# Kernel tuning notes

Measured on AMD Instinct MI355X. Metric: run time of the kernel, lower is better.

Reference implementation:

```python
import jax, jax.numpy as jnp
import numpy as np

# Dimensions (production-scale Qwen3-MoE-like, scaled for CPU exec)
T = 1024   # num_tokens
H = 1024   # hidden_size
F = 768    # moe_inter_padding_size (per-expert ffn dim)
E = 32     # expert_num (== num_local_experts, ep_size=1 -> expert_map is identity)
K = 4      # moe_k (top-k)


def setup_inputs() -> dict:
    key = jax.random.key(0)
    k1, k2, k3, k4 = jax.random.split(key, 4)
    hidden_states = jax.random.normal(k1, (T, H), jnp.float32)
    gate_w = jax.random.normal(k2, (E, H), jnp.float32) * 0.02       # router Linear weight (out,in)
    w1 = jax.random.normal(k3, (E, 2 * F, H), jnp.float32) * 0.02    # fused gate+up proj per expert
    w2 = jax.random.normal(k4, (E, H, F), jnp.float32) * 0.02        # down proj per expert
    return {"hidden_states": hidden_states, "gate_w": gate_w, "w1": w1, "w2": w2}


def reference(hidden_states, gate_w, w1, w2):
    # Router gate (logits computed in fp32, as in the torch code)
    router_logits = (hidden_states @ gate_w.T).astype(jnp.float32)      # [T, E]
    probs = jax.nn.softmax(router_logits, axis=-1)                      # [T, E]
    # SelectTopkOp: top-k over softmax probs, renormalize selected weights
    topk_w, topk_ids = jax.lax.top_k(probs, K)                          # [T, K]
    topk_w = topk_w / jnp.sum(topk_w, axis=-1, keepdims=True)
    # Dense combine weights: cw[t, e] = sum_k topk_w[t, k] * [topk_ids[t, k] == e]
    onehot = jax.nn.one_hot(topk_ids, E, dtype=topk_w.dtype)            # [T, K, E]
    cw = jnp.einsum("tk,tke->te", topk_w, onehot)                       # [T, E]
    # Grouped expert MLP with SiGLU: silu(gate) * up, then down proj
    gu = jnp.einsum("th,egh->etg", hidden_states, w1)                   # [E, T, 2F]
    g, u = gu[..., :F], gu[..., F:]
    act = jax.nn.silu(g) * u                                            # [E, T, F]
    y = jnp.einsum("etf,ehf->eth", act, w2)                             # [E, T, H]
    # Combine: weight each expert's output by its (sparse) routing weight
    out = jnp.einsum("eth,te->th", y, cw.astype(y.dtype))               # [T, H]
    return out
```

## Files before the change

kernel.cpp:

```cpp
#include <hip/hip_runtime.h>
#include <hip/hip_bf16.h>
#include <cmath>

#define TT 1024
#define HH 1024
#define FF 768
#define EE 32
#define MAXTILE 96

typedef __bf16 bf16;
typedef __bf16 v4bf __attribute__((ext_vector_type(4)));
typedef __bf16 v8bf __attribute__((ext_vector_type(8)));
typedef float  v4f  __attribute__((ext_vector_type(4)));

static __device__ __forceinline__ v4f mfma16(v8bf a, v8bf b, v4f c) {
    return __builtin_amdgcn_mfma_f32_16x16x32_bf16(a, b, c, 0, 0, 0);
}

__global__ __launch_bounds__(64) void router_k(
    const float* __restrict__ x, const float* __restrict__ gw,
    bf16* __restrict__ xbf, int* __restrict__ tk_id, float* __restrict__ tk_w)
{
    int t = blockIdx.x, lane = threadIdx.x;
    float4 xr[4];
    const float4* xrow = (const float4*)(x + (size_t)t * HH);
#pragma unroll
    for (int i = 0; i < 4; ++i) xr[i] = xrow[i * 64 + lane];
#pragma unroll
    for (int i = 0; i < 4; ++i) {
        v4bf b = { (bf16)xr[i].x, (bf16)xr[i].y, (bf16)xr[i].z, (bf16)xr[i].w };
        *(v4bf*)(xbf + (size_t)t * HH + (i * 64 + lane) * 4) = b;
    }

    double acc[EE];
#pragma unroll
    for (int e = 0; e < EE; ++e) {
        const float4* grow = (const float4*)(gw + (size_t)e * HH);
        double a = 0.0;
#pragma unroll
        for (int i = 0; i < 4; ++i) {
            float4 g = grow[i * 64 + lane];
            a += (double)xr[i].x * g.x + (double)xr[i].y * g.y
               + (double)xr[i].z * g.z + (double)xr[i].w * g.w;
        }
        acc[e] = a;
    }
#pragma unroll
    for (int m = 1; m < 64; m <<= 1) {
#pragma unroll
        for (int e = 0; e < EE; ++e) acc[e] += __shfl_xor(acc[e], m, 64);
    }
    if (lane == 0) {
        int ids[4]; double lv[4];
        for (int k = 0; k < 4; ++k) {
            int best = 0; double bv = -1.0e300;
            for (int e = 0; e < EE; ++e)
                if (acc[e] > bv) { bv = acc[e]; best = e; }
            ids[k] = best; lv[k] = bv; acc[best] = -2.0e300;
        }
        double w[4], s = 0.0;
        for (int k = 0; k < 4; ++k) { w[k] = exp(lv[k] - lv[0]); s += w[k]; }
        for (int k = 0; k < 4; ++k) {
            tk_id[t * 4 + k] = ids[k];
            tk_w[t * 4 + k] = (float)(w[k] / s);
        }
    }
}

__global__ __launch_bounds__(1024) void scatter_k(
    const int* __restrict__ tk_id, const float* __restrict__ tk_w,
    int* __restrict__ cnt, int* __restrict__ offs,
    int* __restrict__ list, float* __restrict__ wlist,
    int* __restrict__ tile_e, int* __restrict__ tile_m)
{
    __shared__ int c_s[EE], o_s[EE], cur_s[EE];
    int tid = threadIdx.x;
    if (tid < EE) { c_s[tid] = 0; cur_s[tid] = 0; }
    __syncthreads();
    int ids[4]; float w[4];
#pragma unroll
    for (int k = 0; k < 4; ++k) { ids[k] = tk_id[tid * 4 + k]; w[k] = tk_w[tid * 4 + k]; }
#pragma unroll
    for (int k = 0; k < 4; ++k) atomicAdd(&c_s[ids[k]], 1);
    __syncthreads();
    if (tid == 0) {
        int a = 0;
        for (int e = 0; e < EE; ++e) { o_s[e] = a; a += c_s[e]; }
        int nt = 0;
        for (int e = 0; e < EE; ++e)
            for (int m = 0; m * 64 < c_s[e]; ++m) { tile_e[nt] = e; tile_m[nt] = m; ++nt; }
        for (int i = nt; i < MAXTILE; ++i) { tile_e[i] = -1; tile_m[i] = 0; }
    }
    __syncthreads();
#pragma unroll
    for (int k = 0; k < 4; ++k) {
        int e = ids[k];
        int pos = atomicAdd(&cur_s[e], 1);
        int idx = o_s[e] + pos;
        list[idx] = tid * 4 + k;
        wlist[idx] = w[k];
    }
    if (tid < EE) { cnt[tid] = c_s[tid]; offs[tid] = o_s[tid]; }
    if (tid >= 1024 - 64) {
        list[4096 + (tid - 960)] = 0;
        wlist[4096 + (tid - 960)] = 0.f;
    }
}

__global__ __launch_bounds__(256) void gemm1_k(
    const bf16* __restrict__ xbf, const float* __restrict__ w1,
    const int* __restrict__ cnt, const int* __restrict__ offs,
    const int* __restrict__ list, const int* __restrict__ tile_e,
    const int* __restrict__ tile_m, bf16* __restrict__ act)
{
    int id = blockIdx.x;
    int p = (id & 7) * 144 + (id >> 3);
    int fb = p / MAXTILE, tl = p % MAXTILE;
    int e = tile_e[tl];
    if (e < 0) return;
    int mt = tile_m[tl];
    int n = cnt[e];
    int base = offs[e];

    __shared__ bf16 As[64][72];
    __shared__ bf16 Bs[128][72];

    int tid = threadIdx.x;
    int wid = tid >> 6, lane = tid & 63;
    int wr = wid >> 1, wc = wid & 1;
    int lrow = lane & 15, lk = (lane >> 4) * 8;
    const float* w1e = w1 + (size_t)e * 1536 * HH;

    int r0 = tid >> 3, r1 = 32 + (tid >> 3), oct = tid & 7;
    int tk0 = list[base + mt * 64 + r0] >> 2;
    int tk1 = list[base + mt * 64 + r1] >> 2;

    v4f accg[2][2], accu[2][2];
#pragma unroll
    for (int m = 0; m < 2; ++m)
#pragma unroll
        for (int nf = 0; nf < 2; ++nf) { accg[m][nf] = (v4f)0.f; accu[m][nf] = (v4f)0.f; }

    for (int k0 = 0; k0 < HH; k0 += 64) {
        *(v8bf*)&As[r0][oct * 8] = *(const v8bf*)(xbf + (size_t)tk0 * HH + k0 + oct * 8);
        *(v8bf*)&As[r1][oct * 8] = *(const v8bf*)(xbf + (size_t)tk1 * HH + k0 + oct * 8);
#pragma unroll
        for (int it = 0; it < 8; ++it) {
            int r = it * 16 + (tid >> 4);
            int q = tid & 15;
            int grow = (r < 64) ? (fb * 64 + r) : (768 + fb * 64 + (r - 64));
            float4 v = *(const float4*)(w1e + (size_t)grow * HH + k0 + q * 4);
            bf16* dst = &Bs[r][q * 4];
            dst[0] = (bf16)v.x; dst[1] = (bf16)v.y;
            dst[2] = (bf16)v.z; dst[3] = (bf16)v.w;
        }
        __syncthreads();
#pragma unroll
        for (int ks = 0; ks < 2; ++ks) {
            int kk = ks * 32 + lk;
            v8bf a0  = *(const v8bf*)&As[wr * 32 + lrow][kk];
            v8bf a1  = *(const v8bf*)&As[wr * 32 + 16 + lrow][kk];
            v8bf bg0 = *(const v8bf*)&Bs[wc * 32 + lrow][kk];
            v8bf bg1 = *(const v8bf*)&Bs[wc * 32 + 16 + lrow][kk];
            v8bf bu0 = *(const v8bf*)&Bs[64 + wc * 32 + lrow][kk];
            v8bf bu1 = *(const v8bf*)&Bs[64 + wc * 32 + 16 + lrow][kk];
            accg[0][0] = mfma16(a0, bg0, accg[0][0]);
            accg[0][1] = mfma16(a0, bg1, accg[0][1]);
            accg[1][0] = mfma16(a1, bg0, accg[1][0]);
            accg[1][1] = mfma16(a1, bg1, accg[1][1]);
            accu[0][0] = mfma16(a0, bu0, accu[0][0]);
            accu[0][1] = mfma16(a0, bu1, accu[0][1]);
            accu[1][0] = mfma16(a1, bu0, accu[1][0]);
            accu[1][1] = mfma16(a1, bu1, accu[1][1]);
        }
        __syncthreads();
    }
    int rb = wr * 32 + (lane >> 4) * 4;
#pragma unroll
    for (int m = 0; m < 2; ++m)
#pragma unroll
        for (int nf = 0; nf < 2; ++nf)
#pragma unroll
            for (int j = 0; j < 4; ++j) {
                int r = mt * 64 + rb + m * 16 + j;
                if (r < n) {
                    float g = accg[m][nf][j], u = accu[m][nf][j];
                    float a = g / (1.f + __expf(-g)) * u;
                    act[(size_t)(base + r) * FF + fb * 64 + wc * 32 + nf * 16 + lrow] = (bf16)a;
                }
            }
}

__global__ __launch_bounds__(256) void gemm2_k(
    const bf16* __restrict__ act, const float* __restrict__ w2,
    const int* __restrict__ cnt, const int* __restrict__ offs,
    const int* __restrict__ list, const float* __restrict__ wlist,
    const int* __restrict__ tile_e, const int* __restrict__ tile_m,
    float* __restrict__ ybuf)
{
    int id = blockIdx.x;
    int p = (id & 7) * 192 + (id >> 3);
    int hb = p / MAXTILE, tl = p % MAXTILE;
    int e = tile_e[tl];
    if (e < 0) return;
    int mt = tile_m[tl];
    int n = cnt[e];
    int base = offs[e];

    __shared__ bf16 As[64][72];
    __shared__ bf16 Bs[64][72];

    int tid = threadIdx.x;
    int wid = tid >> 6, lane = tid & 63;
    int wr = wid >> 1, wc = wid & 1;
    int lrow = lane & 15, lk = (lane >> 4) * 8;
    const float* w2e = w2 + (size_t)e * HH * FF;

    int r0 = tid >> 3, r1 = 32 + (tid >> 3), oct = tid & 7;
    const bf16* arow0 = act + (size_t)(base + mt * 64 + r0) * FF;
    const bf16* arow1 = act + (size_t)(base + mt * 64 + r1) * FF;

    v4f acc[2][2];
#pragma unroll
    for (int m = 0; m < 2; ++m)
#pragma unroll
        for (int nf = 0; nf < 2; ++nf) acc[m][nf] = (v4f)0.f;

    for (int k0 = 0; k0 < FF; k0 += 64) {
        *(v8bf*)&As[r0][oct * 8] = *(const v8bf*)(arow0 + k0 + oct * 8);
        *(v8bf*)&As[r1][oct * 8] = *(const v8bf*)(arow1 + k0 + oct * 8);
#pragma unroll
        for (int it = 0; it < 4; ++it) {
            int r = it * 16 + (tid >> 4);
            int q = tid & 15;
            float4 v = *(const float4*)(w2e + (size_t)(hb * 64 + r) * FF + k0 + q * 4);
            bf16* dst = &Bs[r][q * 4];
            dst[0] = (bf16)v.x; dst[1] = (bf16)v.y;
            dst[2] = (bf16)v.z; dst[3] = (bf16)v.w;
        }
        __syncthreads();
#pragma unroll
        for (int ks = 0; ks < 2; ++ks) {
            int kk = ks * 32 + lk;
            v8bf a0 = *(const v8bf*)&As[wr * 32 + lrow][kk];
            v8bf a1 = *(const v8bf*)&As[wr * 32 + 16 + lrow][kk];
            v8bf b0 = *(const v8bf*)&Bs[wc * 32 + lrow][kk];
            v8bf b1 = *(const v8bf*)&Bs[wc * 32 + 16 + lrow][kk];
            acc[0][0] = mfma16(a0, b0, acc[0][0]);
            acc[0][1] = mfma16(a0, b1, acc[0][1]);
            acc[1][0] = mfma16(a1, b0, acc[1][0]);
            acc[1][1] = mfma16(a1, b1, acc[1][1]);
        }
        __syncthreads();
    }
    int rb = wr * 32 + (lane >> 4) * 4;
#pragma unroll
    for (int m = 0; m < 2; ++m)
#pragma unroll
        for (int j = 0; j < 4; ++j) {
            int r = mt * 64 + rb + m * 16 + j;
            if (r < n) {
                int code = list[base + r];
                float w = wlist[base + r];
#pragma unroll
                for (int nf = 0; nf < 2; ++nf) {
                    int col = wc * 32 + nf * 16 + lrow;
                    ybuf[(size_t)code * HH + hb * 64 + col] = acc[m][nf][j] * w;
                }
            }
        }
}

__global__ __launch_bounds__(256) void combine_k(
    const float* __restrict__ ybuf, float* __restrict__ out)
{
    int idx = blockIdx.x * 256 + threadIdx.x;
    int t = idx >> 8, c = idx & 255;
    const float4* yb = (const float4*)ybuf;
    float4 a = yb[(size_t)(t * 4 + 0) * 256 + c];
    float4 b = yb[(size_t)(t * 4 + 1) * 256 + c];
    float4 d = yb[(size_t)(t * 4 + 2) * 256 + c];
    float4 e = yb[(size_t)(t * 4 + 3) * 256 + c];
    float4 s;
    s.x = a.x + b.x + d.x + e.x;
    s.y = a.y + b.y + d.y + e.y;
    s.z = a.z + b.z + d.z + e.z;
    s.w = a.w + b.w + d.w + e.w;
    ((float4*)out)[(size_t)t * 256 + c] = s;
}

extern "C" void kernel_launch(void* const* d_in, const int* in_sizes, int n_in,
                              void* d_out, int out_size, void* d_ws, size_t ws_size,
                              hipStream_t stream)
{
    const float* x  = (const float*)d_in[0];
    const float* gw = (const float*)d_in[1];
    const float* w1 = (const float*)d_in[2];
    const float* w2 = (const float*)d_in[3];
    float* out = (float*)d_out;

    char* ws = (char*)d_ws;
    size_t off = 0;
    auto alloc = [&](size_t bytes) {
        void* p = ws + off;
        off = (off + bytes + 255) & ~(size_t)255;
        return p;
    };
    bf16*  xbf    = (bf16*) alloc((size_t)TT * HH * 2);
    int*   tk_id  = (int*)  alloc(4096 * 4);
    float* tk_w   = (float*)alloc(4096 * 4);
    int*   cnt    = (int*)  alloc(EE * 4);
    int*   offs   = (int*)  alloc(EE * 4);
    int*   list   = (int*)  alloc(4160 * 4);
    float* wlist  = (float*)alloc(4160 * 4);
    int*   tile_e = (int*)  alloc(MAXTILE * 4);
    int*   tile_m = (int*)  alloc(MAXTILE * 4);
    bf16*  act    = (bf16*) alloc((size_t)4160 * FF * 2);
    float* ybuf   = (float*)alloc((size_t)4096 * HH * 4);

    router_k<<<TT, 64, 0, stream>>>(x, gw, xbf, tk_id, tk_w);
    scatter_k<<<1, 1024, 0, stream>>>(tk_id, tk_w, cnt, offs, list, wlist, tile_e, tile_m);
    gemm1_k<<<MAXTILE * 12, 256, 0, stream>>>(xbf, w1, cnt, offs, list, tile_e, tile_m, act);
    gemm2_k<<<MAXTILE * 16, 256, 0, stream>>>(act, w2, cnt, offs, list, wlist, tile_e, tile_m, ybuf);
    combine_k<<<1024, 256, 0, stream>>>(ybuf, out);
}
```

Before: 482.2 us.

## Prefetch next K-tile into registers, reorder tile mapping, atomic-add combine into output

Both grouped GEMMs now load the next K-slice of activations and weights into registers before running the MFMAs on the current slice, then write it to shared memory, so global load latency overlaps compute. The block-to-tile mapping changes so that consecutive blocks share the same expert tile and sweep its F/H column blocks instead of the reverse. The per-slot ybuf plus combine kernel is replaced by zeroing the output and having gemm2 atomically add weighted results into it, which removes a large intermediate write and read but introduces atomic contention and non-deterministic summation order.

```diff
diff --git a/kernel.cpp b/kernel.cpp
--- a/kernel.cpp
+++ b/kernel.cpp
@@ -15,6 +15,11 @@
 
 static __device__ __forceinline__ v4f mfma16(v8bf a, v8bf b, v4f c) {
     return __builtin_amdgcn_mfma_f32_16x16x32_bf16(a, b, c, 0, 0, 0);
+}
+
+__global__ __launch_bounds__(256) void zero_k(float4* __restrict__ out4)
+{
+    out4[(size_t)blockIdx.x * 256 + threadIdx.x] = float4{0.f, 0.f, 0.f, 0.f};
 }
 
 __global__ __launch_bounds__(64) void router_k(
@@ -115,7 +120,7 @@
 {
     int id = blockIdx.x;
     int p = (id & 7) * 144 + (id >> 3);
-    int fb = p / MAXTILE, tl = p % MAXTILE;
+    int tl = p / 12, fb = p % 12;
     int e = tile_e[tl];
     if (e < 0) return;
     int mt = tile_m[tl];
@@ -132,8 +137,34 @@
     const float* w1e = w1 + (size_t)e * 1536 * HH;
 
     int r0 = tid >> 3, r1 = 32 + (tid >> 3), oct = tid & 7;
-    int tk0 = list[base + mt * 64 + r0] >> 2;
-    int tk1 = list[base + mt * 64 + r1] >> 2;
+    const bf16* aptr0 = xbf + (size_t)(list[base + mt * 64 + r0] >> 2) * HH + oct * 8;
+    const bf16* aptr1 = xbf + (size_t)(list[base + mt * 64 + r1] >> 2) * HH + oct * 8;
+    int brow = tid >> 4, bq = tid & 15;
+
+    v8bf a_r0, a_r1;
+    float4 b_r[8];
+
+    auto issue = [&](int k0) {
+        a_r0 = *(const v8bf*)(aptr0 + k0);
+        a_r1 = *(const v8bf*)(aptr1 + k0);
+#pragma unroll
+        for (int it = 0; it < 8; ++it) {
+            int r = it * 16 + brow;
+            int grow = (r < 64) ? (fb * 64 + r) : (768 + fb * 64 + (r - 64));
+            b_r[it] = *(const float4*)(w1e + (size_t)grow * HH + k0 + bq * 4);
+        }
+    };
+    auto commit = [&]() {
+        *(v8bf*)&As[r0][oct * 8] = a_r0;
+        *(v8bf*)&As[r1][oct * 8] = a_r1;
+#pragma unroll
+        for (int it = 0; it < 8; ++it) {
+            int r = it * 16 + brow;
+            bf16* dst = &Bs[r][bq * 4];
+            dst[0] = (bf16)b_r[it].x; dst[1] = (bf16)b_r[it].y;
+            dst[2] = (bf16)b_r[it].z; dst[3] = (bf16)b_r[it].w;
+        }
+    };
 
     v4f accg[2][2], accu[2][2];
 #pragma unroll
@@ -141,20 +172,13 @@
 #pragma unroll
         for (int nf = 0; nf < 2; ++nf) { accg[m][nf] = (v4f)0.f; accu[m][nf] = (v4f)0.f; }
 
+    issue(0);
+    commit();
+    __syncthreads();
+
     for (int k0 = 0; k0 < HH; k0 += 64) {
-        *(v8bf*)&As[r0][oct * 8] = *(const v8bf*)(xbf + (size_t)tk0 * HH + k0 + oct * 8);
-        *(v8bf*)&As[r1][oct * 8] = *(const v8bf*)(xbf + (size_t)tk1 * HH + k0 + oct * 8);
-#pragma unroll
-        for (int it = 0; it < 8; ++it) {
-            int r = it * 16 + (tid >> 4);
-            int q = tid & 15;
-            int grow = (r < 64) ? (fb * 64 + r) : (768 + fb * 64 + (r - 64));
-            float4 v = *(const float4*)(w1e + (size_t)grow * HH + k0 + q * 4);
-            bf16* dst = &Bs[r][q * 4];
-            dst[0] = (bf16)v.x; dst[1] = (bf16)v.y;
-            dst[2] = (bf16)v.z; dst[3] = (bf16)v.w;
-        }
-        __syncthreads();
+        int kn = (k0 + 64 < HH) ? (k0 + 64) : k0;
+        issue(kn);
 #pragma unroll
         for (int ks = 0; ks < 2; ++ks) {
             int kk = ks * 32 + lk;
@@ -174,6 +198,8 @@
             accu[1][1] = mfma16(a1, bu1, accu[1][1]);
         }
         __syncthreads();
+        commit();
+        __syncthreads();
     }
     int rb = wr * 32 + (lane >> 4) * 4;
 #pragma unroll
@@ -196,11 +222,11 @@
     const int* __restrict__ cnt, const int* __restrict__ offs,
     const int* __restrict__ list, const float* __restrict__ wlist,
     const int* __restrict__ tile_e, const int* __restrict__ tile_m,
-    float* __restrict__ ybuf)
+    float* __restrict__ out)
 {
     int id = blockIdx.x;
     int p = (id & 7) * 192 + (id >> 3);
-    int hb = p / MAXTILE, tl = p % MAXTILE;
+    int tl = p / 16, hb = p % 16;
     int e = tile_e[tl];
     if (e < 0) return;
     int mt = tile_m[tl];
@@ -217,8 +243,33 @@
     const float* w2e = w2 + (size_t)e * HH * FF;
 
     int r0 = tid >> 3, r1 = 32 + (tid >> 3), oct = tid & 7;
-    const bf16* arow0 = act + (size_t)(base + mt * 64 + r0) * FF;
-    const bf16* arow1 = act + (size_t)(base + mt * 64 + r1) * FF;
+    const bf16* arow0 = act + (size_t)(base + mt * 64 + r0) * FF + oct * 8;
+    const bf16* arow1 = act + (size_t)(base + mt * 64 + r1) * FF + oct * 8;
+    int brow = tid >> 4, bq = tid & 15;
+
+    v8bf a_r0, a_r1;
+    float4 b_r[4];
+
+    auto issue = [&](int k0) {
+        a_r0 = *(const v8bf*)(arow0 + k0);
+        a_r1 = *(const v8bf*)(arow1 + k0);
+#pragma unroll
+        for (int it = 0; it < 4; ++it) {
+            int r = it * 16 + brow;
+            b_r[it] = *(const float4*)(w2e + (size_t)(hb * 64 + r) * FF + k0 + bq * 4);
+        }
+    };
+    auto commit = [&]() {
+        *(v8bf*)&As[r0][oct * 8] = a_r0;
+        *(v8bf*)&As[r1][oct * 8] = a_r1;
+#pragma unroll
+        for (int it = 0; it < 4; ++it) {
+            int r = it * 16 + brow;
+            bf16* dst = &Bs[r][bq * 4];
+            dst[0] = (bf16)b_r[it].x; dst[1] = (bf16)b_r[it].y;
+            dst[2] = (bf16)b_r[it].z; dst[3] = (bf16)b_r[it].w;
+        }
+    };
 
     v4f acc[2][2];
 #pragma unroll
@@ -226,19 +277,13 @@
 #pragma unroll
         for (int nf = 0; nf < 2; ++nf) acc[m][nf] = (v4f)0.f;
 
+    issue(0);
+    commit();
+    __syncthreads();
+
     for (int k0 = 0; k0 < FF; k0 += 64) {
-        *(v8bf*)&As[r0][oct * 8] = *(const v8bf*)(arow0 + k0 + oct * 8);
-        *(v8bf*)&As[r1][oct * 8] = *(const v8bf*)(arow1 + k0 + oct * 8);
-#pragma unroll
-        for (int it = 0; it < 4; ++it) {
-            int r = it * 16 + (tid >> 4);
-            int q = tid & 15;
-            float4 v = *(const float4*)(w2e + (size_t)(hb * 64 + r) * FF + k0 + q * 4);
-            bf16* dst = &Bs[r][q * 4];
-            dst[0] = (bf16)v.x; dst[1] = (bf16)v.y;
-            dst[2] = (bf16)v.z; dst[3] = (bf16)v.w;
-        }
-        __syncthreads();
+        int kn = (k0 + 64 < FF) ? (k0 + 64) : k0;
+        issue(kn);
 #pragma unroll
         for (int ks = 0; ks < 2; ++ks) {
             int kk = ks * 32 + lk;
@@ -252,6 +297,8 @@
             acc[1][1] = mfma16(a1, b1, acc[1][1]);
         }
         __syncthreads();
+        commit();
+        __syncthreads();
     }
     int rb = wr * 32 + (lane >> 4) * 4;
 #pragma unroll
@@ -260,33 +307,15 @@
         for (int j = 0; j < 4; ++j) {
             int r = mt * 64 + rb + m * 16 + j;
             if (r < n) {
-                int code = list[base + r];
+                int tk = list[base + r] >> 2;
                 float w = wlist[base + r];
 #pragma unroll
                 for (int nf = 0; nf < 2; ++nf) {
                     int col = wc * 32 + nf * 16 + lrow;
-                    ybuf[(size_t)code * HH + hb * 64 + col] = acc[m][nf][j] * w;
+                    atomicAdd(out + (size_t)tk * HH + hb * 64 + col, acc[m][nf][j] * w);
                 }
             }
         }
-}
-
-__global__ __launch_bounds__(256) void combine_k(
-    const float* __restrict__ ybuf, float* __restrict__ out)
-{
-    int idx = blockIdx.x * 256 + threadIdx.x;
-    int t = idx >> 8, c = idx & 255;
-    const float4* yb = (const float4*)ybuf;
-    float4 a = yb[(size_t)(t * 4 + 0) * 256 + c];
-    float4 b = yb[(size_t)(t * 4 + 1) * 256 + c];
-    float4 d = yb[(size_t)(t * 4 + 2) * 256 + c];
-    float4 e = yb[(size_t)(t * 4 + 3) * 256 + c];
-    float4 s;
-    s.x = a.x + b.x + d.x + e.x;
-    s.y = a.y + b.y + d.y + e.y;
-    s.z = a.z + b.z + d.z + e.z;
-    s.w = a.w + b.w + d.w + e.w;
-    ((float4*)out)[(size_t)t * 256 + c] = s;
 }
 
 extern "C" void kernel_launch(void* const* d_in, const int* in_sizes, int n_in,
@@ -316,11 +345,10 @@
     int*   tile_e = (int*)  alloc(MAXTILE * 4);
     int*   tile_m = (int*)  alloc(MAXTILE * 4);
     bf16*  act    = (bf16*) alloc((size_t)4160 * FF * 2);
-    float* ybuf   = (float*)alloc((size_t)4096 * HH * 4);
-
+
+    zero_k<<<1024, 256, 0, stream>>>((float4*)out);
     router_k<<<TT, 64, 0, stream>>>(x, gw, xbf, tk_id, tk_w);
     scatter_k<<<1, 1024, 0, stream>>>(tk_id, tk_w, cnt, offs, list, wlist, tile_e, tile_m);
     gemm1_k<<<MAXTILE * 12, 256, 0, stream>>>(xbf, w1, cnt, offs, list, tile_e, tile_m, act);
-    gemm2_k<<<MAXTILE * 16, 256, 0, stream>>>(act, w2, cnt, offs, list, wlist, tile_e, tile_m, ybuf);
-    combine_k<<<1024, 256, 0, stream>>>(ybuf, out);
-}
+    gemm2_k<<<MAXTILE * 16, 256, 0, stream>>>(act, w2, cnt, offs, list, wlist, tile_e, tile_m, out);
+}
```

After: 500.9 us. 3.9% more time.

## Enlarge token tiles to 128 rows so each fp32 weight tile is reused more

Applied to the files above, without the earlier changes.

Token tiles per expert grow from 64 to 128 rows, so each converted fp32 weight slice is shared by twice as many tokens and total weight traffic and bf16 conversion drop. gemm1 narrows its F slice from 64 to 32 columns, giving 24 F blocks that each load and convert half as much weight per tile. Both GEMMs switch to wider vectorized loads and packed 16-byte LDS stores for the weight conversion. The cost is more padded rows in partly filled tiles for experts with few tokens, and fewer active tiles per block.

```diff
diff --git a/kernel.cpp b/kernel.cpp
--- a/kernel.cpp
+++ b/kernel.cpp
@@ -6,7 +6,7 @@
 #define HH 1024
 #define FF 768
 #define EE 32
-#define MAXTILE 96
+#define MAXT2 64
 
 typedef __bf16 bf16;
 typedef __bf16 v4bf __attribute__((ext_vector_type(4)));
@@ -88,8 +88,8 @@
         for (int e = 0; e < EE; ++e) { o_s[e] = a; a += c_s[e]; }
         int nt = 0;
         for (int e = 0; e < EE; ++e)
-            for (int m = 0; m * 64 < c_s[e]; ++m) { tile_e[nt] = e; tile_m[nt] = m; ++nt; }
-        for (int i = nt; i < MAXTILE; ++i) { tile_e[i] = -1; tile_m[i] = 0; }
+            for (int m = 0; m * 128 < c_s[e]; ++m) { tile_e[nt] = e; tile_m[nt] = m; ++nt; }
+        for (int i = nt; i < MAXT2; ++i) { tile_e[i] = -1; tile_m[i] = 0; }
     }
     __syncthreads();
 #pragma unroll
@@ -101,9 +101,9 @@
         wlist[idx] = w[k];
     }
     if (tid < EE) { cnt[tid] = c_s[tid]; offs[tid] = o_s[tid]; }
-    if (tid >= 1024 - 64) {
-        list[4096 + (tid - 960)] = 0;
-        wlist[4096 + (tid - 960)] = 0.f;
+    if (tid >= 1024 - 128) {
+        list[4096 + (tid - 896)] = 0;
+        wlist[4096 + (tid - 896)] = 0.f;
     }
 }
 
@@ -114,16 +114,16 @@
     const int* __restrict__ tile_m, bf16* __restrict__ act)
 {
     int id = blockIdx.x;
-    int p = (id & 7) * 144 + (id >> 3);
-    int fb = p / MAXTILE, tl = p % MAXTILE;
+    int p = (id & 7) * 192 + (id >> 3);
+    int fb = p >> 6, tl = p & 63;
     int e = tile_e[tl];
     if (e < 0) return;
     int mt = tile_m[tl];
     int n = cnt[e];
     int base = offs[e];
 
-    __shared__ bf16 As[64][72];
-    __shared__ bf16 Bs[128][72];
+    __shared__ bf16 As[128][72];
+    __shared__ bf16 Bs[64][72];
 
     int tid = threadIdx.x;
     int wid = tid >> 6, lane = tid & 63;
@@ -131,64 +131,58 @@
     int lrow = lane & 15, lk = (lane >> 4) * 8;
     const float* w1e = w1 + (size_t)e * 1536 * HH;
 
-    int r0 = tid >> 3, r1 = 32 + (tid >> 3), oct = tid & 7;
-    int tk0 = list[base + mt * 64 + r0] >> 2;
-    int tk1 = list[base + mt * 64 + r1] >> 2;
-
-    v4f accg[2][2], accu[2][2];
-#pragma unroll
-    for (int m = 0; m < 2; ++m)
-#pragma unroll
-        for (int nf = 0; nf < 2; ++nf) { accg[m][nf] = (v4f)0.f; accu[m][nf] = (v4f)0.f; }
+    int arow = tid >> 1, ahalf = (tid & 1) * 32;
+    const bf16* aptr = xbf + (size_t)(list[base + mt * 128 + arow] >> 2) * HH + ahalf;
+    int brow = tid >> 2, bq = (tid & 3) * 16;
+    int grow = (brow < 32) ? (fb * 32 + brow) : (FF + fb * 32 + (brow - 32));
+    const float* bptr = w1e + (size_t)grow * HH + bq;
+
+    v4f accg[4], accu[4];
+#pragma unroll
+    for (int m = 0; m < 4; ++m) { accg[m] = (v4f)0.f; accu[m] = (v4f)0.f; }
 
     for (int k0 = 0; k0 < HH; k0 += 64) {
-        *(v8bf*)&As[r0][oct * 8] = *(const v8bf*)(xbf + (size_t)tk0 * HH + k0 + oct * 8);
-        *(v8bf*)&As[r1][oct * 8] = *(const v8bf*)(xbf + (size_t)tk1 * HH + k0 + oct * 8);
-#pragma unroll
-        for (int it = 0; it < 8; ++it) {
-            int r = it * 16 + (tid >> 4);
-            int q = tid & 15;
-            int grow = (r < 64) ? (fb * 64 + r) : (768 + fb * 64 + (r - 64));
-            float4 v = *(const float4*)(w1e + (size_t)grow * HH + k0 + q * 4);
-            bf16* dst = &Bs[r][q * 4];
-            dst[0] = (bf16)v.x; dst[1] = (bf16)v.y;
-            dst[2] = (bf16)v.z; dst[3] = (bf16)v.w;
-        }
+#pragma unroll
+        for (int q = 0; q < 4; ++q)
+            *(v8bf*)&As[arow][ahalf + q * 8] = *(const v8bf*)(aptr + k0 + q * 8);
+        float4 f0 = *(const float4*)(bptr + k0);
+        float4 f1 = *(const float4*)(bptr + k0 + 4);
+        float4 f2 = *(const float4*)(bptr + k0 + 8);
+        float4 f3 = *(const float4*)(bptr + k0 + 12);
+        v8bf p0 = { (bf16)f0.x, (bf16)f0.y, (bf16)f0.z, (bf16)f0.w,
+                    (bf16)f1.x, (bf16)f1.y, (bf16)f1.z, (bf16)f1.w };
+        v8bf p1 = { (bf16)f2.x, (bf16)f2.y, (bf16)f2.z, (bf16)f2.w,
+                    (bf16)f3.x, (bf16)f3.y, (bf16)f3.z, (bf16)f3.w };
+        *(v8bf*)&Bs[brow][bq] = p0;
+        *(v8bf*)&Bs[brow][bq + 8] = p1;
         __syncthreads();
 #pragma unroll
         for (int ks = 0; ks < 2; ++ks) {
             int kk = ks * 32 + lk;
-            v8bf a0  = *(const v8bf*)&As[wr * 32 + lrow][kk];
-            v8bf a1  = *(const v8bf*)&As[wr * 32 + 16 + lrow][kk];
-            v8bf bg0 = *(const v8bf*)&Bs[wc * 32 + lrow][kk];
-            v8bf bg1 = *(const v8bf*)&Bs[wc * 32 + 16 + lrow][kk];
-            v8bf bu0 = *(const v8bf*)&Bs[64 + wc * 32 + lrow][kk];
-            v8bf bu1 = *(const v8bf*)&Bs[64 + wc * 32 + 16 + lrow][kk];
-            accg[0][0] = mfma16(a0, bg0, accg[0][0]);
-            accg[0][1] = mfma16(a0, bg1, accg[0][1]);
-            accg[1][0] = mfma16(a1, bg0, accg[1][0]);
-            accg[1][1] = mfma16(a1, bg1, accg[1][1]);
-            accu[0][0] = mfma16(a0, bu0, accu[0][0]);
-            accu[0][1] = mfma16(a0, bu1, accu[0][1]);
-            accu[1][0] = mfma16(a1, bu0, accu[1][0]);
-            accu[1][1] = mfma16(a1, bu1, accu[1][1]);
+            v8bf bg = *(const v8bf*)&Bs[wc * 16 + lrow][kk];
+            v8bf bu = *(const v8bf*)&Bs[32 + wc * 16 + lrow][kk];
+#pragma unroll
+            for (int mi = 0; mi < 4; ++mi) {
+                v8bf a = *(const v8bf*)&As[wr * 64 + mi * 16 + lrow][kk];
+                accg[mi] = mfma16(a, bg, accg[mi]);
+                accu[mi] = mfma16(a, bu, accu[mi]);
+            }
         }
         __syncthreads();
     }
-    int rb = wr * 32 + (lane >> 4) * 4;
-#pragma unroll
-    for (int m = 0; m < 2; ++m)
-#pragma unroll
-        for (int nf = 0; nf < 2; ++nf)
-#pragma unroll
-            for (int j = 0; j < 4; ++j) {
-                int r = mt * 64 + rb + m * 16 + j;
-                if (r < n) {
-                    float g = accg[m][nf][j], u = accu[m][nf][j];
-                    float a = g / (1.f + __expf(-g)) * u;
-                    act[(size_t)(base + r) * FF + fb * 64 + wc * 32 + nf * 16 + lrow] = (bf16)a;
-                }
+    int rsub = (lane >> 4) * 4;
+    int col = fb * 32 + wc * 16 + lrow;
+#pragma unroll
+    for (int mi = 0; mi < 4; ++mi)
+#pragma unroll
+        for (int j = 0; j < 4; ++j) {
+            int r = mt * 128 + wr * 64 + mi * 16 + rsub + j;
+            if (r < n) {
+                float g = accg[mi][j], u = accu[mi][j];
+                float a = g / (1.f + __expf(-g)) * u;
+                act[(size_t)(base + r) * FF + col] = (bf16)a;
             }
+        }
 }
 
 __global__ __launch_bounds__(256) void gemm2_k(
@@ -199,15 +193,15 @@
     float* __restrict__ ybuf)
 {
     int id = blockIdx.x;
-    int p = (id & 7) * 192 + (id >> 3);
-    int hb = p / MAXTILE, tl = p % MAXTILE;
+    int p = (id & 7) * 128 + (id >> 3);
+    int hb = p >> 6, tl = p & 63;
     int e = tile_e[tl];
     if (e < 0) return;
     int mt = tile_m[tl];
     int n = cnt[e];
     int base = offs[e];
 
-    __shared__ bf16 As[64][72];
+    __shared__ bf16 As[128][72];
     __shared__ bf16 Bs[64][72];
 
     int tid = threadIdx.x;
@@ -216,56 +210,59 @@
     int lrow = lane & 15, lk = (lane >> 4) * 8;
     const float* w2e = w2 + (size_t)e * HH * FF;
 
-    int r0 = tid >> 3, r1 = 32 + (tid >> 3), oct = tid & 7;
-    const bf16* arow0 = act + (size_t)(base + mt * 64 + r0) * FF;
-    const bf16* arow1 = act + (size_t)(base + mt * 64 + r1) * FF;
-
-    v4f acc[2][2];
-#pragma unroll
-    for (int m = 0; m < 2; ++m)
+    int arow = tid >> 1, ahalf = (tid & 1) * 32;
+    const bf16* aptr = act + (size_t)(base + mt * 128 + arow) * FF + ahalf;
+    int brow = tid >> 2, bq = (tid & 3) * 16;
+    const float* bptr = w2e + (size_t)(hb * 64 + brow) * FF + bq;
+
+    v4f acc[4][2];
+#pragma unroll
+    for (int m = 0; m < 4; ++m)
 #pragma unroll
         for (int nf = 0; nf < 2; ++nf) acc[m][nf] = (v4f)0.f;
 
     for (int k0 = 0; k0 < FF; k0 += 64) {
-        *(v8bf*)&As[r0][oct * 8] = *(const v8bf*)(arow0 + k0 + oct * 8);
-        *(v8bf*)&As[r1][oct * 8] = *(const v8bf*)(arow1 + k0 + oct * 8);
-#pragma unroll
-        for (int it = 0; it < 4; ++it) {
-            int r = it * 16 + (tid >> 4);
-            int q = tid & 15;
-            float4 v = *(const float4*)(w2e + (size_t)(hb * 64 + r) * FF + k0 + q * 4);
-            bf16* dst = &Bs[r][q * 4];
-            dst[0] = (bf16)v.x; dst[1] = (bf16)v.y;
-            dst[2] = (bf16)v.z; dst[3] = (bf16)v.w;
-        }
+#pragma unroll
+        for (int q = 0; q < 4; ++q)
+            *(v8bf*)&As[arow][ahalf + q * 8] = *(const v8bf*)(aptr + k0 + q * 8);
+        float4 f0 = *(const float4*)(bptr + k0);
+        float4 f1 = *(const float4*)(bptr + k0 + 4);
+        float4 f2 = *(const float4*)(bptr + k0 + 8);
+        float4 f3 = *(const float4*)(bptr + k0 + 12);
+        v8bf p0 = { (bf16)f0.x, (bf16)f0.y, (bf16)f0.z, (bf16)f0.w,
+                    (bf16)f1.x, (bf16)f1.y, (bf16)f1.z, (bf16)f1.w };
+        v8bf p1 = { (bf16)f2.x, (bf16)f2.y, (bf16)f2.z, (bf16)f2.w,
+                    (bf16)f3.x, (bf16)f3.y, (bf16)f3.z, (bf16)f3.w };
+        *(v8bf*)&Bs[brow][bq] = p0;
+        *(v8bf*)&Bs[brow][bq + 8] = p1;
         __syncthreads();
 #pragma unroll
         for (int ks = 0; ks < 2; ++ks) {
             int kk = ks * 32 + lk;
-            v8bf a0 = *(const v8bf*)&As[wr * 32 + lrow][kk];
-            v8bf a1 = *(const v8bf*)&As[wr * 32 + 16 + lrow][kk];
             v8bf b0 = *(const v8bf*)&Bs[wc * 32 + lrow][kk];
             v8bf b1 = *(const v8bf*)&Bs[wc * 32 + 16 + lrow][kk];
-            acc[0][0] = mfma16(a0, b0, acc[0][0]);
-            acc[0][1] = mfma16(a0, b1, acc[0][1]);
-            acc[1][0] = mfma16(a1, b0, acc[1][0]);
-            acc[1][1] = mfma16(a1, b1, acc[1][1]);
+#pragma unroll
+            for (int mi = 0; mi < 4; ++mi) {
+                v8bf a = *(const v8bf*)&As[wr * 64 + mi * 16 + lrow][kk];
+                acc[mi][0] = mfma16(a, b0, acc[mi][0]);
+                acc[mi][1] = mfma16(a, b1, acc[mi][1]);
+            }
         }
         __syncthreads();
     }
-    int rb = wr * 32 + (lane >> 4) * 4;
-#pragma unroll
-    for (int m = 0; m < 2; ++m)
+    int rsub = (lane >> 4) * 4;
+#pragma unroll
+    for (int mi = 0; mi < 4; ++mi)
 #pragma unroll
         for (int j = 0; j < 4; ++j) {
-            int r = mt * 64 + rb + m * 16 + j;
+            int r = mt * 128 + wr * 64 + mi * 16 + rsub + j;
             if (r < n) {
                 int code = list[base + r];
                 float w = wlist[base + r];
 #pragma unroll
                 for (int nf = 0; nf < 2; ++nf) {
-                    int col = wc * 32 + nf * 16 + lrow;
-                    ybuf[(size_t)code * HH + hb * 64 + col] = acc[m][nf][j] * w;
+                    int col = hb * 64 + wc * 32 + nf * 16 + lrow;
+                    ybuf[(size_t)code * HH + col] = acc[mi][nf][j] * w;
                 }
             }
         }
@@ -311,16 +308,16 @@
     float* tk_w   = (float*)alloc(4096 * 4);
     int*   cnt    = (int*)  alloc(EE * 4);
     int*   offs   = (int*)  alloc(EE * 4);
-    int*   list   = (int*)  alloc(4160 * 4);
-    float* wlist  = (float*)alloc(4160 * 4);
-    int*   tile_e = (int*)  alloc(MAXTILE * 4);
-    int*   tile_m = (int*)  alloc(MAXTILE * 4);
-    bf16*  act    = (bf16*) alloc((size_t)4160 * FF * 2);
+    int*   list   = (int*)  alloc(4224 * 4);
+    float* wlist  = (float*)alloc(4224 * 4);
+    int*   tile_e = (int*)  alloc(MAXT2 * 4);
+    int*   tile_m = (int*)  alloc(MAXT2 * 4);
+    bf16*  act    = (bf16*) alloc((size_t)4224 * FF * 2);
     float* ybuf   = (float*)alloc((size_t)4096 * HH * 4);
 
     router_k<<<TT, 64, 0, stream>>>(x, gw, xbf, tk_id, tk_w);
     scatter_k<<<1, 1024, 0, stream>>>(tk_id, tk_w, cnt, offs, list, wlist, tile_e, tile_m);
-    gemm1_k<<<MAXTILE * 12, 256, 0, stream>>>(xbf, w1, cnt, offs, list, tile_e, tile_m, act);
-    gemm2_k<<<MAXTILE * 16, 256, 0, stream>>>(act, w2, cnt, offs, list, wlist, tile_e, tile_m, ybuf);
+    gemm1_k<<<1536, 256, 0, stream>>>(xbf, w1, cnt, offs, list, tile_e, tile_m, act);
+    gemm2_k<<<1024, 256, 0, stream>>>(act, w2, cnt, offs, list, wlist, tile_e, tile_m, ybuf);
     combine_k<<<1024, 256, 0, stream>>>(ybuf, out);
 }
```

Result: slower. 521.6 us (+8.2%).
